# Kernel optimization log

Hardware: AMD Instinct MI355X
Metric: run time of the kernel (lower is better)

Reference implementation:

```python
import jax, jax.numpy as jnp
import numpy as np


def setup_inputs() -> dict:
    key = jax.random.key(0)
    ks = jax.random.split(key, 8)
    T, B, D = 2048, 8, 1024
    d, NM, k = 64, 8, 2
    Mp1 = NM + 1
    s_in = 1.0 / np.sqrt(D)
    X = jax.random.normal(ks[0], (T, B, D), dtype=jnp.float32)
    M0 = 0.02 * jax.random.normal(ks[1], (d, d), dtype=jnp.float32)
    W_q = s_in * jax.random.normal(ks[2], (D, d), dtype=jnp.float32)
    b_q = jnp.zeros((d,), jnp.float32)
    W_k = s_in * jax.random.normal(ks[3], (D, Mp1 * d), dtype=jnp.float32)
    b_k = jnp.zeros((Mp1 * d,), jnp.float32)
    W_v = s_in * jax.random.normal(ks[4], (D, Mp1 * d), dtype=jnp.float32)
    b_v = jnp.zeros((Mp1 * d,), jnp.float32)
    W_g = s_in * jax.random.normal(ks[5], (D, NM), dtype=jnp.float32)
    b_g = jnp.zeros((NM,), jnp.float32)
    return dict(X=X, M0=M0, W_q=W_q, b_q=b_q, W_k=W_k, b_k=b_k,
                W_v=W_v, b_v=b_v, W_g=W_g, b_g=b_g, k=k)


def _mom_forward(X, M0, W_q, b_q, W_k, b_k, W_v, b_v, W_g, b_g, k):
    T, B, D = X.shape
    d = M0.shape[0]
    NM = W_g.shape[1]
    Mp1 = NM + 1  # memory 0 is the always-on shared memory
    Kp1 = k + 1
    # --- gating + top-k memory selection ---
    scores = jax.nn.softmax(X @ W_g + b_g, axis=-1)               # (T,B,NM)
    m_sc, m_idx = jax.lax.top_k(scores, k)                        # (T,B,k)
    m_sc = m_sc / jnp.sum(m_sc, axis=-1, keepdims=True)
    m_idx = m_idx + 1                                             # shift: 0 reserved for shared memory
    idx_u = jnp.concatenate([jnp.zeros((T, B, 1), m_idx.dtype), m_idx], axis=2)  # (T,B,Kp1)
    sc_u = jnp.concatenate([jnp.ones((T, B, 1), m_sc.dtype), m_sc], axis=2)      # (T,B,Kp1)
    # --- varlen pack: sort replicated tokens by (batch, memory, time) ---
    # NB: the torch build_varlen_pack runs under @torch.no_grad -> detached
    t_rep = jnp.broadcast_to(jnp.arange(T)[:, None, None], (T, B, Kp1)).reshape(-1)
    b_rep = jnp.broadcast_to(jnp.arange(B)[None, :, None], (T, B, Kp1)).reshape(-1)
    m_rep = idx_u.reshape(-1)
    sort_key = b_rep * (Mp1 * T) + m_rep * T + t_rep              # unique per packed token
    perm = jnp.argsort(sort_key)
    t_o = t_rep[perm]
    b_o = b_rep[perm]
    m_id = m_rep[perm]
    alpha = jax.lax.stop_gradient(sc_u.reshape(-1)[perm])         # (Tt,)
    x_tilde = jax.lax.stop_gradient(
        jnp.broadcast_to(X[:, :, None, :], (T, B, Kp1, D)).reshape(-1, D)[perm])  # (Tt,D)
    Tt = T * B * Kp1
    # segment id per packed token; state resets at each new (batch, memory) segment
    seg = b_o * Mp1 + m_id
    new_seg = jnp.concatenate([jnp.ones((1,), bool), seg[1:] != seg[:-1]])
    # --- projections; pick k/v head matching each token's routed memory ---
    q_t = x_tilde @ W_q + b_q                                     # (Tt,d)
    K_all = (x_tilde @ W_k + b_k).reshape(Tt, Mp1, d)
    V_all = (x_tilde @ W_v + b_v).reshape(Tt, Mp1, d)
    k_t = jnp.take_along_axis(K_all, m_id[:, None, None], axis=1)[:, 0]  # (Tt,d)
    v_t = jnp.take_along_axis(V_all, m_id[:, None, None], axis=1)[:, 0]  # (Tt,d)
    # --- per-segment linear-attention recurrence: M_t = M0 + sum k_tau v_tau^T, o_t = q_t @ M_t ---
    def step(M, inp):
        qt, kt, vt, ns = inp
        M = jnp.where(ns, M0, M)
        M = M + kt[:, None] * vt[None, :]
        return M, qt @ M
    _, o_tilde = jax.lax.scan(step, M0, (q_t, k_t, v_t, new_seg))  # (Tt,d)
    # --- weighted scatter-add back to (T,B,d) ---
    o = jnp.zeros((T, B, d), X.dtype).at[t_o, b_o].add(alpha[:, None] * o_tilde)
    return o


def reference(X, M0, W_q, b_q, W_k, b_k, W_v, b_v, W_g, b_g, k):
    return _mom_forward(X, M0, W_q, b_q, W_k, b_k, W_v, b_v, W_g, b_g, k)
```

## Files before the change

### kernel.cpp

```cpp
#include <hip/hip_runtime.h>

#define TT   2048
#define BB   8
#define DD   1024
#define HD   64
#define MP1  9
#define NTOK (TT*BB)
#define CH   64
#define NC   32
#define NSEG (BB*MP1)
#define SEGCAP 2048
#define NCAT 1280
#define LDP  72
#define NZB  1024

typedef __attribute__((ext_vector_type(8))) short bf16x8;
typedef __attribute__((ext_vector_type(4))) float f32x4;

union U8 { uint4 v; unsigned short s[8]; };

static __device__ __forceinline__ unsigned short f2bf(float f) {
  union { float f; unsigned u; } c; c.f = f;
  unsigned r = (c.u + 0x7FFF + ((c.u >> 16) & 1)) >> 16;
  return (unsigned short)r;
}
static __device__ __forceinline__ float bf2f(unsigned short s) {
  union { unsigned u; float f; } c; c.u = ((unsigned)s) << 16;
  return c.f;
}

static __device__ __forceinline__ int sched_walk(
    const int* __restrict__ seglen, int bid, int* chunk_out) {
  const int batch = bid & 7;
  int idx = bid >> 3;
  for (int m = 0; m < MP1; m++) {
    int nch = (seglen[batch * MP1 + m] + 63) >> 6;
    if (idx < nch) { *chunk_out = idx; return batch * MP1 + m; }
    idx -= nch;
  }
  return -1;
}

__global__ __launch_bounds__(256) void prep(
    const float* __restrict__ X,
    const float* __restrict__ Wq, const float* __restrict__ Wk,
    const float* __restrict__ Wv, const float* __restrict__ bq,
    const float* __restrict__ bk, const float* __restrict__ bv,
    const float* __restrict__ Wg, const float* __restrict__ bg,
    unsigned short* __restrict__ Wt, float* __restrict__ bcat,
    int2* __restrict__ idxb, float2* __restrict__ alfb,
    unsigned short* __restrict__ Xb,
    float4* __restrict__ outz, int n4) {
  __shared__ float smem[8 * DD];
  const int tid = threadIdx.x;
  const int id = blockIdx.x;
  if (id >= 1344) {
    int i = (id - 1344) * 256 + tid;
    if (i < n4) outz[i] = make_float4(0.f, 0.f, 0.f, 0.f);
    return;
  }
  if (id < 320) {
    float (*tile)[65] = (float(*)[65])smem;
    const int n0 = (id % 20) * 64, k0 = (id / 20) * 64;
    const int c = tid & 63, rr = tid >> 6;
#pragma unroll 4
    for (int i = 0; i < 16; i++) {
      int kk = k0 + rr * 16 + i;
      int n  = n0 + c;
      float v = 0.f;
      if (n0 < 64)        v = Wq[kk * 64 + n];
      else if (n0 < 640)  v = Wk[kk * 576 + (n - 64)];
      else if (n0 < 1216) v = Wv[kk * 576 + (n - 640)];
      tile[rr * 16 + i][c] = v;
    }
    __syncthreads();
    const int lk = (tid & 15) * 4, ln = tid >> 4;
#pragma unroll
    for (int p = 0; p < 4; p++) {
      int nl = p * 16 + ln;
      ushort4 o;
      o.x = f2bf(tile[lk + 0][nl]); o.y = f2bf(tile[lk + 1][nl]);
      o.z = f2bf(tile[lk + 2][nl]); o.w = f2bf(tile[lk + 3][nl]);
      *(ushort4*)&Wt[(size_t)(n0 + nl) * DD + k0 + lk] = o;
    }
    if (id == 0) {
      for (int idx = tid; idx < NCAT; idx += 256) {
        float b = 0.f;
        if (idx < 64)        b = bq[idx];
        else if (idx < 640)  b = bk[idx - 64];
        else if (idx < 1216) b = bv[idx - 640];
        bcat[idx] = b;
      }
    }
    return;
  }
  float* wgT = smem;
#pragma unroll
  for (int idx4 = tid; idx4 < 2048; idx4 += 256) {
    float4 v = *(const float4*)&Wg[(size_t)idx4 * 4];
    int flat = idx4 * 4;
    int i = flat >> 3, j = flat & 7;
    wgT[(j + 0) * DD + i] = v.x;
    wgT[(j + 1) * DD + i] = v.y;
    wgT[(j + 2) * DD + i] = v.z;
    wgT[(j + 3) * DD + i] = v.w;
  }
  __syncthreads();
  const int lane = tid & 63, wave = tid >> 6;
  const int base_tok = (id - 320) * 16 + wave * 4;
  for (int tk = 0; tk < 4; tk++) {
    const int tok = base_tok + tk;
    const float* xr = X + (size_t)tok * DD;
    unsigned short* xbr = Xb + ((size_t)((tok & 7) * TT + (tok >> 3))) * DD;
    float p[8] = {0.f,0.f,0.f,0.f,0.f,0.f,0.f,0.f};
#pragma unroll
    for (int it = 0; it < 4; it++) {
      int i = it * 256 + lane * 4;
      float4 x = *(const float4*)&xr[i];
      ushort4 o;
      o.x = f2bf(x.x); o.y = f2bf(x.y); o.z = f2bf(x.z); o.w = f2bf(x.w);
      *(ushort4*)&xbr[i] = o;
#pragma unroll
      for (int j = 0; j < 8; j++) {
        float4 wv = *(const float4*)&wgT[j * DD + i];
        p[j] += x.x * wv.x + x.y * wv.y + x.z * wv.z + x.w * wv.w;
      }
    }
#pragma unroll
    for (int j = 0; j < 8; j++) {
      float v = p[j];
#pragma unroll
      for (int off = 32; off > 0; off >>= 1) v += __shfl_xor(v, off);
      p[j] = v + bg[j];
    }
    if (lane == 0) {
      int i1 = 0; float z1 = p[0];
#pragma unroll
      for (int j = 1; j < 8; j++) if (p[j] > z1) { z1 = p[j]; i1 = j; }
      int i2 = -1; float z2 = -3.0e38f;
#pragma unroll
      for (int j = 0; j < 8; j++) if (j != i1 && p[j] > z2) { z2 = p[j]; i2 = j; }
      float e   = expf(z2 - z1);
      float inv = 1.0f / (1.0f + e);
      idxb[tok] = make_int2(i1 + 1, i2 + 1);
      alfb[tok] = make_float2(inv, e * inv);
    }
  }
}

__global__ __launch_bounds__(1024) void pack_kernel(
    const int2* __restrict__ idxb, const float2* __restrict__ alfb,
    int* __restrict__ tlist, float* __restrict__ alist,
    int* __restrict__ seglen) {
  const int seg = blockIdx.x;
  const int b = seg / MP1, m = seg % MP1;
  const int tid = threadIdx.x;
  int* tl = tlist + (size_t)seg * SEGCAP;
  float* al = alist + (size_t)seg * SEGCAP;
  if (m == 0) {
    for (int pos = tid; pos < TT; pos += 1024) { tl[pos] = pos; al[pos] = 1.f; }
    if (tid == 0) seglen[seg] = TT;
    return;
  }
  __shared__ int wsum[16];
  const int lane = tid & 63, w = tid >> 6;
  int base = 0;
  for (int r = 0; r < TT / 1024; r++) {
    int t = r * 1024 + tid;
    int2 ix = idxb[t * BB + b];
    bool f = (ix.x == m || ix.y == m);
    float2 af = alfb[t * BB + b];
    float alpha = (ix.x == m) ? af.x : af.y;
    unsigned long long mask = __ballot(f);
    int lanepos = __popcll(mask & ((1ull << lane) - 1ull));
    if (lane == 0) wsum[w] = __popcll(mask);
    __syncthreads();
    int wbase = 0, total = 0;
#pragma unroll
    for (int i = 0; i < 16; i++) { int v = wsum[i]; if (i < w) wbase += v; total += v; }
    if (f) { int pos = base + wbase + lanepos; tl[pos] = t; al[pos] = alpha; }
    base += total;
    __syncthreads();
  }
  if (tid == 0) seglen[seg] = base;
  int Lpad = (base + 63) & ~63;
  for (int pos = base + tid; pos < Lpad; pos += 1024) { tl[pos] = 0; al[pos] = 0.f; }
}

#define ABUF_H 4096
#define BBUF_H 12288

template<bool DOQ>
static __device__ __forceinline__ void pkv_body(
    const unsigned short* __restrict__ Xb, const unsigned short* __restrict__ Wt,
    const float* __restrict__ bcat, const int* __restrict__ tlist,
    unsigned short* __restrict__ KVseg, unsigned short* __restrict__ Qd,
    unsigned short* Asb, unsigned short* Bsb, int* tls,
    int seg, int t0) {
  const int b = seg / MP1, m = seg % MP1;
  const int tid = threadIdx.x;
  const int lane = tid & 63, w = tid >> 6;
  if (tid < 64) tls[tid] = tlist[(size_t)seg * SEGCAP + t0 + tid];
  __syncthreads();

  const int lrow = lane >> 2;
  const int lk   = (lane & 3) * 8;
  const unsigned short* aPtr = Xb + ((size_t)b * TT + tls[w * 16 + lrow]) * DD + lk;
  const unsigned short* kPtr = Wt + (size_t)(64  + m * 64 + w * 16 + lrow) * DD + lk;
  const unsigned short* vPtr = Wt + (size_t)(640 + m * 64 + w * 16 + lrow) * DD + lk;
  const unsigned short* qPtr = Wt + (size_t)(w * 16 + lrow) * DD + lk;

  const int wr = (w >> 1) * 32;
  const int wc64 = (w & 1);
  const int quad = lane >> 4, l15 = lane & 15;

  float biasv[4], qbias[2];
#pragma unroll
  for (int n = 0; n < 4; n++) {
    int col = wc64 * 64 + n * 16 + l15;
    biasv[n] = bcat[col < 64 ? (64 + m * 64 + col) : (640 + m * 64 + (col - 64))];
  }
  if (DOQ) {
#pragma unroll
    for (int i = 0; i < 2; i++) qbias[i] = bcat[wc64 * 32 + i * 16 + l15];
  } else { qbias[0] = 0.f; qbias[1] = 0.f; }
  asm volatile("s_waitcnt vmcnt(0)" ::: "memory");
  __builtin_amdgcn_sched_barrier(0);

  f32x4 acc[2][4];
  f32x4 qacc[2][2];
#pragma unroll
  for (int i = 0; i < 2; i++) {
#pragma unroll
    for (int j = 0; j < 4; j++) acc[i][j] = (f32x4){0.f, 0.f, 0.f, 0.f};
#pragma unroll
    for (int j = 0; j < 2; j++) qacc[i][j] = (f32x4){0.f, 0.f, 0.f, 0.f};
  }

#define STG(BUF, K0)                                                             \
  do {                                                                           \
    unsigned short* As_ = Asb + (BUF) * ABUF_H;                                  \
    unsigned short* Bs_ = Bsb + (BUF) * BBUF_H;                                  \
    _Pragma("unroll")                                                            \
    for (int s = 0; s < 2; s++) {                                                \
      __builtin_amdgcn_global_load_lds(                                          \
          (const __attribute__((address_space(1))) unsigned int*)(aPtr + (K0) + s * 32), \
          (__attribute__((address_space(3))) unsigned int*)(As_ + s * 2048 + w * 512),   \
          16, 0, 0);                                                             \
      __builtin_amdgcn_global_load_lds(                                          \
          (const __attribute__((address_space(1))) unsigned int*)(kPtr + (K0) + s * 32), \
          (__attribute__((address_space(3))) unsigned int*)(Bs_ + s * 2048 + w * 512),   \
          16, 0, 0);                                                             \
      __builtin_amdgcn_global_load_lds(                                          \
          (const __attribute__((address_space(1))) unsigned int*)(vPtr + (K0) + s * 32), \
          (__attribute__((address_space(3))) unsigned int*)(Bs_ + 4096 + s * 2048 + w * 512), \
          16, 0, 0);                                                             \
      if (DOQ)                                                                   \
        __builtin_amdgcn_global_load_lds(                                        \
            (const __attribute__((address_space(1))) unsigned int*)(qPtr + (K0) + s * 32), \
            (__attribute__((address_space(3))) unsigned int*)(Bs_ + 8192 + s * 2048 + w * 512), \
            16, 0, 0);                                                           \
    }                                                                            \
  } while (0)

#define CMP(BUF)                                                                 \
  do {                                                                           \
    const unsigned short* As_ = Asb + (BUF) * ABUF_H;                            \
    const unsigned short* Bs_ = Bsb + (BUF) * BBUF_H;                            \
    _Pragma("unroll")                                                            \
    for (int s = 0; s < 2; s++) {                                                \
      bf16x8 af[2], bfr[4];                                                      \
      _Pragma("unroll")                                                          \
      for (int i = 0; i < 2; i++)                                                \
        af[i] = *(const bf16x8*)&As_[s * 2048 + (wr + i * 16 + l15) * 32 + quad * 8]; \
      _Pragma("unroll")                                                          \
      for (int n = 0; n < 4; n++)                                                \
        bfr[n] = *(const bf16x8*)&Bs_[wc64 * 4096 + s * 2048 + (n * 16 + l15) * 32 + quad * 8]; \
      _Pragma("unroll")                                                          \
      for (int mi = 0; mi < 2; mi++)                                             \
        _Pragma("unroll")                                                        \
        for (int ni = 0; ni < 4; ni++)                                           \
          acc[mi][ni] = __builtin_amdgcn_mfma_f32_16x16x32_bf16(af[mi], bfr[ni], acc[mi][ni], 0, 0, 0); \
      if (DOQ) {                                                                 \
        bf16x8 qf[2];                                                            \
        _Pragma("unroll")                                                        \
        for (int i = 0; i < 2; i++)                                              \
          qf[i] = *(const bf16x8*)&Bs_[8192 + s * 2048 + (wc64 * 32 + i * 16 + l15) * 32 + quad * 8]; \
        _Pragma("unroll")                                                        \
        for (int mi = 0; mi < 2; mi++)                                           \
          _Pragma("unroll")                                                      \
          for (int ni = 0; ni < 2; ni++)                                         \
            qacc[mi][ni] = __builtin_amdgcn_mfma_f32_16x16x32_bf16(af[mi], qf[ni], qacc[mi][ni], 0, 0, 0); \
      }                                                                          \
    }                                                                            \
  } while (0)

  STG(0, 0);
  STG(1, 64);
  for (int it = 0; it < 15; it++) {
    if (DOQ) asm volatile("s_waitcnt vmcnt(8)" ::: "memory");
    else     asm volatile("s_waitcnt vmcnt(6)" ::: "memory");
    __builtin_amdgcn_sched_barrier(0);
    asm volatile("s_barrier" ::: "memory");
    CMP(it & 1);
    asm volatile("s_waitcnt lgkmcnt(0)" ::: "memory");
    __builtin_amdgcn_sched_barrier(0);
    asm volatile("s_barrier" ::: "memory");
    if (it < 14) STG(it & 1, (it + 2) * 64);
  }
  asm volatile("s_waitcnt vmcnt(0)" ::: "memory");
  __builtin_amdgcn_sched_barrier(0);
  asm volatile("s_barrier" ::: "memory");
  CMP(1);
#undef STG
#undef CMP

#pragma unroll
  for (int ni = 0; ni < 4; ni++) {
    int col = wc64 * 64 + ni * 16 + l15;
#pragma unroll
    for (int mi = 0; mi < 2; mi++) {
      int p = t0 + wr + mi * 16 + quad * 4;
#pragma unroll
      for (int r = 0; r < 4; r++) {
        float v = acc[mi][ni][r] + biasv[ni];
        KVseg[((size_t)seg * SEGCAP + p + r) * 128 + col] = f2bf(v);
      }
    }
  }
  if (DOQ) {
#pragma unroll
    for (int ni = 0; ni < 2; ni++) {
      int qcol = wc64 * 32 + ni * 16 + l15;
#pragma unroll
      for (int mi = 0; mi < 2; mi++) {
        int pr = wr + mi * 16 + quad * 4;
#pragma unroll
        for (int r = 0; r < 4; r++) {
          int t = tls[pr + r];
          float v = qacc[mi][ni][r] + qbias[ni];
          Qd[(size_t)(t * BB + b) * HD + qcol] = f2bf(v);
        }
      }
    }
  }
}

__global__ __launch_bounds__(256) void pkv_mfma(
    const unsigned short* __restrict__ Xb, const unsigned short* __restrict__ Wt,
    const float* __restrict__ bcat,
    const int* __restrict__ tlist, const int* __restrict__ seglen,
    unsigned short* __restrict__ KVseg, unsigned short* __restrict__ Qd) {
  int chunk;
  const int seg = sched_walk(seglen, blockIdx.x, &chunk);
  if (seg < 0) return;
  const int t0 = chunk * 64;
  __shared__ unsigned short Asb[2 * ABUF_H];
  __shared__ unsigned short Bsb[2 * BBUF_H];
  __shared__ int tls[64];
  if (seg % MP1 == 0)
    pkv_body<true>(Xb, Wt, bcat, tlist, KVseg, Qd, Asb, Bsb, tls, seg, t0);
  else
    pkv_body<false>(Xb, Wt, bcat, tlist, KVseg, Qd, Asb, Bsb, tls, seg, t0);
}

__global__ __launch_bounds__(256) void chunk_intra(
    const unsigned short* __restrict__ Qd, const unsigned short* __restrict__ KVseg,
    const int* __restrict__ tlist, const float* __restrict__ alist,
    const int* __restrict__ seglen,
    unsigned short* __restrict__ Sb16, float* __restrict__ out) {
  int chunk;
  const int seg = sched_walk(seglen, blockIdx.x, &chunk);
  if (seg < 0) return;
  const int L = seglen[seg];
  const int t0 = chunk * CH;
  __shared__ unsigned short Qs[64 * LDP];
  __shared__ unsigned short Ks[64 * LDP];
  __shared__ unsigned short KTs[64 * LDP];
  __shared__ unsigned short VTs[64 * LDP];
  const int b = seg / MP1;
  const int tid = threadIdx.x;
  const int* tl = tlist + (size_t)seg * SEGCAP;
  {
    int row = tid >> 2, c16 = (tid & 3) << 4;
    int pos = t0 + row;
    int t = tl[pos];
    const unsigned short* qb = Qd + (size_t)(t * BB + b) * HD;
    *(uint4*)&Qs[row * LDP + c16]     = *(const uint4*)(qb + c16);
    *(uint4*)&Qs[row * LDP + c16 + 8] = *(const uint4*)(qb + c16 + 8);
    const unsigned short* kvb = KVseg + ((size_t)seg * SEGCAP + pos) * 128;
    U8 k0, k1, v0, v1;
    k0.v = *(const uint4*)(kvb + c16);
    k1.v = *(const uint4*)(kvb + c16 + 8);
    v0.v = *(const uint4*)(kvb + 64 + c16);
    v1.v = *(const uint4*)(kvb + 64 + c16 + 8);
    if (pos >= L) { uint4 z = {0,0,0,0}; k0.v = z; k1.v = z; }
    *(uint4*)&Ks[row * LDP + c16]     = k0.v;
    *(uint4*)&Ks[row * LDP + c16 + 8] = k1.v;
#pragma unroll
    for (int j = 0; j < 8; j++) {
      KTs[(c16 + j) * LDP + row]     = k0.s[j];
      KTs[(c16 + 8 + j) * LDP + row] = k1.s[j];
      VTs[(c16 + j) * LDP + row]     = v0.s[j];
      VTs[(c16 + 8 + j) * LDP + row] = v1.s[j];
    }
  }
  __syncthreads();
  const int lane = tid & 63, w = tid >> 6;
  const int quad = lane >> 4, l15 = lane & 15;
  {
    const unsigned short* arow = &VTs[(w * 16 + l15) * LDP];
    bf16x8 a0 = *(const bf16x8*)(arow + quad * 8);
    bf16x8 a1 = *(const bf16x8*)(arow + 32 + quad * 8);
    unsigned short* Sp = Sb16 + ((size_t)seg * NC + chunk) * 4096;
#pragma unroll
    for (int n = 0; n < 4; n++) {
      const unsigned short* brow = &KTs[(n * 16 + l15) * LDP];
      f32x4 acc = __builtin_amdgcn_mfma_f32_16x16x32_bf16(a0, *(const bf16x8*)(brow + quad * 8),
                                                          (f32x4){0.f,0.f,0.f,0.f}, 0, 0, 0);
      acc = __builtin_amdgcn_mfma_f32_16x16x32_bf16(a1, *(const bf16x8*)(brow + 32 + quad * 8),
                                                    acc, 0, 0, 0);
#pragma unroll
      for (int r = 0; r < 4; r++)
        Sp[(w * 16 + quad * 4 + r) * 64 + n * 16 + l15] = f2bf(acc[r]);
    }
  }
  unsigned short* qrow = &Qs[(w * 16 + l15) * LDP];
  bf16x8 aq0 = *(const bf16x8*)(qrow + quad * 8);
  bf16x8 aq1 = *(const bf16x8*)(qrow + 32 + quad * 8);
  f32x4 pp[4];
#pragma unroll
  for (int n = 0; n < 4; n++) {
    const unsigned short* krow = &Ks[(n * 16 + l15) * LDP];
    pp[n] = __builtin_amdgcn_mfma_f32_16x16x32_bf16(aq0, *(const bf16x8*)(krow + quad * 8),
                                                    (f32x4){0.f,0.f,0.f,0.f}, 0, 0, 0);
    pp[n] = __builtin_amdgcn_mfma_f32_16x16x32_bf16(aq1, *(const bf16x8*)(krow + 32 + quad * 8),
                                                    pp[n], 0, 0, 0);
  }
#pragma unroll
  for (int n = 0; n < 4; n++)
#pragma unroll
    for (int r = 0; r < 4; r++) {
      int i = w * 16 + quad * 4 + r, j = n * 16 + l15;
      Qs[i * LDP + j] = (j <= i) ? f2bf(pp[n][r]) : (unsigned short)0;
    }
  bf16x8 ap0 = *(const bf16x8*)(qrow + quad * 8);
  bf16x8 ap1 = *(const bf16x8*)(qrow + 32 + quad * 8);
  f32x4 po[4];
#pragma unroll
  for (int n = 0; n < 4; n++) {
    const unsigned short* vrow = &VTs[(n * 16 + l15) * LDP];
    po[n] = __builtin_amdgcn_mfma_f32_16x16x32_bf16(ap0, *(const bf16x8*)(vrow + quad * 8),
                                                    (f32x4){0.f,0.f,0.f,0.f}, 0, 0, 0);
    po[n] = __builtin_amdgcn_mfma_f32_16x16x32_bf16(ap1, *(const bf16x8*)(vrow + 32 + quad * 8),
                                                    po[n], 0, 0, 0);
  }
#pragma unroll
  for (int r = 0; r < 4; r++) {
    int pos = t0 + w * 16 + quad * 4 + r;
    if (pos < L) {
      int t = tl[pos];
      float alpha = alist[(size_t)seg * SEGCAP + pos];
#pragma unroll
      for (int n = 0; n < 4; n++)
        atomicAdd(&out[(size_t)(t * BB + b) * HD + n * 16 + l15], alpha * po[n][r]);
    }
  }
}

__global__ __launch_bounds__(256) void scan_kernel(
    const float* __restrict__ M0, const int* __restrict__ seglen,
    unsigned short* __restrict__ Sb16) {
  const int batch = blockIdx.x & 7;
  const int idx = blockIdx.x >> 3;
  const int seg = batch * MP1 + (idx >> 2), slab = idx & 3;
  const int nch = (seglen[seg] + CH - 1) / CH;
  if (nch <= 0) return;
  const int tid = threadIdx.x;
  const int off = slab * 1024 + tid * 4;
  float run[4];
#pragma unroll
  for (int u = 0; u < 4; u++) {
    int o = off + u;
    run[u] = M0[(o & 63) * 64 + (o >> 6)];
  }
  unsigned short* base = Sb16 + (size_t)seg * NC * 4096;
  ushort4 s = *(const ushort4*)(base + off);
  for (int c = 0; c < nch; c++) {
    unsigned short* p = base + c * 4096 + off;
    ushort4 snext;
    if (c + 1 < nch) snext = *(const ushort4*)(p + 4096);
    ushort4 o;
    o.x = f2bf(run[0]); o.y = f2bf(run[1]); o.z = f2bf(run[2]); o.w = f2bf(run[3]);
    *(ushort4*)p = o;
    run[0] += bf2f(s.x); run[1] += bf2f(s.y); run[2] += bf2f(s.z); run[3] += bf2f(s.w);
    s = snext;
  }
}

__global__ __launch_bounds__(256) void chunk_inter(
    const unsigned short* __restrict__ Qd, const unsigned short* __restrict__ Sb16,
    const int* __restrict__ tlist, const float* __restrict__ alist,
    const int* __restrict__ seglen, float* __restrict__ out) {
  int chunk;
  const int seg = sched_walk(seglen, blockIdx.x, &chunk);
  if (seg < 0) return;
  const int L = seglen[seg];
  const int t0 = chunk * CH;
  __shared__ unsigned short Qs[64 * LDP];
  __shared__ unsigned short MT[64 * LDP];
  const int b = seg / MP1;
  const int tid = threadIdx.x;
  const int* tl = tlist + (size_t)seg * SEGCAP;
  {
    int row = tid >> 2, c16 = (tid & 3) << 4;
    int pos = t0 + row;
    const unsigned short* qb = Qd + (size_t)(tl[pos] * BB + b) * HD;
    *(uint4*)&Qs[row * LDP + c16]     = *(const uint4*)(qb + c16);
    *(uint4*)&Qs[row * LDP + c16 + 8] = *(const uint4*)(qb + c16 + 8);
    const unsigned short* Mp = Sb16 + ((size_t)seg * NC + chunk) * 4096 + row * 64 + c16;
    *(uint4*)&MT[row * LDP + c16]     = *(const uint4*)(Mp);
    *(uint4*)&MT[row * LDP + c16 + 8] = *(const uint4*)(Mp + 8);
  }
  __syncthreads();
  const int lane = tid & 63, w = tid >> 6;
  const int quad = lane >> 4, l15 = lane & 15;
  const unsigned short* qrow = &Qs[(w * 16 + l15) * LDP];
  bf16x8 aq0 = *(const bf16x8*)(qrow + quad * 8);
  bf16x8 aq1 = *(const bf16x8*)(qrow + 32 + quad * 8);
  f32x4 po[4];
#pragma unroll
  for (int n = 0; n < 4; n++) {
    const unsigned short* mrow = &MT[(n * 16 + l15) * LDP];
    po[n] = __builtin_amdgcn_mfma_f32_16x16x32_bf16(aq0, *(const bf16x8*)(mrow + quad * 8),
                                                    (f32x4){0.f,0.f,0.f,0.f}, 0, 0, 0);
    po[n] = __builtin_amdgcn_mfma_f32_16x16x32_bf16(aq1, *(const bf16x8*)(mrow + 32 + quad * 8),
                                                    po[n], 0, 0, 0);
  }
#pragma unroll
  for (int r = 0; r < 4; r++) {
    int pos = t0 + w * 16 + quad * 4 + r;
    if (pos < L) {
      int t = tl[pos];
      float alpha = alist[(size_t)seg * SEGCAP + pos];
#pragma unroll
      for (int n = 0; n < 4; n++)
        atomicAdd(&out[(size_t)(t * BB + b) * HD + n * 16 + l15], alpha * po[n][r]);
    }
  }
}

extern "C" void kernel_launch(void* const* d_in, const int* in_sizes, int n_in,
                              void* d_out, int out_size, void* d_ws, size_t ws_size,
                              hipStream_t stream) {
  const float* X  = (const float*)d_in[0];
  const float* M0 = (const float*)d_in[1];
  const float* Wq = (const float*)d_in[2];
  const float* bq = (const float*)d_in[3];
  const float* Wk = (const float*)d_in[4];
  const float* bk = (const float*)d_in[5];
  const float* Wv = (const float*)d_in[6];
  const float* bv = (const float*)d_in[7];
  const float* Wg = (const float*)d_in[8];
  const float* bg = (const float*)d_in[9];

  char* ws = (char*)d_ws;
  unsigned short* Xb   = (unsigned short*)(ws);
  unsigned short* Wt   = (unsigned short*)(ws + 33554432ULL);
  float*          bcat = (float*)         (ws + 36175872ULL);
  unsigned short* Qd   = (unsigned short*)(ws + 36180992ULL);
  unsigned short* KVsg = (unsigned short*)(ws + 38278144ULL);
  unsigned short* Sb16 = (unsigned short*)(ws + 76026880ULL);
  int2*           idxb = (int2*)          (ws + 94901248ULL);
  float2*         alfb = (float2*)        (ws + 95032320ULL);
  int*            tlist= (int*)           (ws + 95163392ULL);
  float*          alist= (float*)         (ws + 95753216ULL);
  int*            slen = (int*)           (ws + 96343040ULL);

  float* out = (float*)d_out;
  const int n4 = out_size / 4;

  prep<<<320 + NTOK / 16 + NZB, 256, 0, stream>>>(
      X, Wq, Wk, Wv, bq, bk, bv, Wg, bg, Wt, bcat, idxb, alfb, Xb,
      (float4*)out, n4);
  pack_kernel<<<NSEG, 1024, 0, stream>>>(idxb, alfb, tlist, alist, slen);
  pkv_mfma<<<1024, 256, 0, stream>>>(Xb, Wt, bcat, tlist, slen, KVsg, Qd);
  chunk_intra<<<1024, 256, 0, stream>>>(Qd, KVsg, tlist, alist, slen, Sb16, out);
  scan_kernel<<<288, 256, 0, stream>>>(M0, slen, Sb16);
  chunk_inter<<<1024, 256, 0, stream>>>(Qd, Sb16, tlist, alist, slen, out);
}
```

Before: 112.4 us.

## Fuse K/V/Q projection into intra-chunk attention kernel, drop KV global round trip

Merges the projection kernel and the intra-chunk kernel into one, so projected K, V and Q tiles go straight from MFMA accumulators into shared memory instead of through a global KV buffer. Every segment now computes the Q projection locally, which adds Q-weight loads and MFMAs for non-shared memories, and Q is still written to global only for memory 0. This removes one launch and the KV write/read traffic, but raises per-block work and LDS reuse pressure.

```diff
diff --git a/kernel.cpp b/kernel.cpp
--- a/kernel.cpp
+++ b/kernel.cpp
@@ -190,14 +190,23 @@
 #define ABUF_H 4096
 #define BBUF_H 12288
 
-template<bool DOQ>
-static __device__ __forceinline__ void pkv_body(
+__global__ __launch_bounds__(256) void pkv_intra(
     const unsigned short* __restrict__ Xb, const unsigned short* __restrict__ Wt,
-    const float* __restrict__ bcat, const int* __restrict__ tlist,
-    unsigned short* __restrict__ KVseg, unsigned short* __restrict__ Qd,
-    unsigned short* Asb, unsigned short* Bsb, int* tls,
-    int seg, int t0) {
+    const float* __restrict__ bcat,
+    const int* __restrict__ tlist, const float* __restrict__ alist,
+    const int* __restrict__ seglen,
+    unsigned short* __restrict__ Sb16, unsigned short* __restrict__ Qd,
+    float* __restrict__ out) {
+  int chunk;
+  const int seg = sched_walk(seglen, blockIdx.x, &chunk);
+  if (seg < 0) return;
+  const int t0 = chunk * 64;
+  const int L = seglen[seg];
   const int b = seg / MP1, m = seg % MP1;
+  __shared__ unsigned short lds[2 * (ABUF_H + BBUF_H)];
+  __shared__ int tls[64];
+  unsigned short* Asb = lds;
+  unsigned short* Bsb = lds + 2 * ABUF_H;
   const int tid = threadIdx.x;
   const int lane = tid & 63, w = tid >> 6;
   if (tid < 64) tls[tid] = tlist[(size_t)seg * SEGCAP + t0 + tid];
@@ -220,10 +229,8 @@
     int col = wc64 * 64 + n * 16 + l15;
     biasv[n] = bcat[col < 64 ? (64 + m * 64 + col) : (640 + m * 64 + (col - 64))];
   }
-  if (DOQ) {
-#pragma unroll
-    for (int i = 0; i < 2; i++) qbias[i] = bcat[wc64 * 32 + i * 16 + l15];
-  } else { qbias[0] = 0.f; qbias[1] = 0.f; }
+#pragma unroll
+  for (int i = 0; i < 2; i++) qbias[i] = bcat[wc64 * 32 + i * 16 + l15];
   asm volatile("s_waitcnt vmcnt(0)" ::: "memory");
   __builtin_amdgcn_sched_barrier(0);
 
@@ -255,11 +262,10 @@
           (const __attribute__((address_space(1))) unsigned int*)(vPtr + (K0) + s * 32), \
           (__attribute__((address_space(3))) unsigned int*)(Bs_ + 4096 + s * 2048 + w * 512), \
           16, 0, 0);                                                             \
-      if (DOQ)                                                                   \
-        __builtin_amdgcn_global_load_lds(                                        \
-            (const __attribute__((address_space(1))) unsigned int*)(qPtr + (K0) + s * 32), \
-            (__attribute__((address_space(3))) unsigned int*)(Bs_ + 8192 + s * 2048 + w * 512), \
-            16, 0, 0);                                                           \
+      __builtin_amdgcn_global_load_lds(                                          \
+          (const __attribute__((address_space(1))) unsigned int*)(qPtr + (K0) + s * 32), \
+          (__attribute__((address_space(3))) unsigned int*)(Bs_ + 8192 + s * 2048 + w * 512), \
+          16, 0, 0);                                                             \
     }                                                                            \
   } while (0)
 
@@ -281,7 +287,7 @@
         _Pragma("unroll")                                                        \
         for (int ni = 0; ni < 4; ni++)                                           \
           acc[mi][ni] = __builtin_amdgcn_mfma_f32_16x16x32_bf16(af[mi], bfr[ni], acc[mi][ni], 0, 0, 0); \
-      if (DOQ) {                                                                 \
+      {                                                                          \
         bf16x8 qf[2];                                                            \
         _Pragma("unroll")                                                        \
         for (int i = 0; i < 2; i++)                                              \
@@ -298,8 +304,7 @@
   STG(0, 0);
   STG(1, 64);
   for (int it = 0; it < 15; it++) {
-    if (DOQ) asm volatile("s_waitcnt vmcnt(8)" ::: "memory");
-    else     asm volatile("s_waitcnt vmcnt(6)" ::: "memory");
+    asm volatile("s_waitcnt vmcnt(8)" ::: "memory");
     __builtin_amdgcn_sched_barrier(0);
     asm volatile("s_barrier" ::: "memory");
     CMP(it & 1);
@@ -315,99 +320,51 @@
 #undef STG
 #undef CMP
 
+  asm volatile("s_waitcnt lgkmcnt(0)" ::: "memory");
+  __builtin_amdgcn_sched_barrier(0);
+  __syncthreads();
+
+  unsigned short* Qs  = lds;
+  unsigned short* Ks  = lds + 64 * LDP;
+  unsigned short* KTs = lds + 2 * 64 * LDP;
+  unsigned short* VTs = lds + 3 * 64 * LDP;
+
+#pragma unroll
+  for (int ni = 0; ni < 2; ni++) {
+    int qcol = wc64 * 32 + ni * 16 + l15;
+#pragma unroll
+    for (int mi = 0; mi < 2; mi++) {
+#pragma unroll
+      for (int r = 0; r < 4; r++) {
+        int pr = wr + mi * 16 + quad * 4 + r;
+        unsigned short qv = f2bf(qacc[mi][ni][r] + qbias[ni]);
+        Qs[pr * LDP + qcol] = qv;
+        if (m == 0) Qd[(size_t)((t0 + pr) * BB + b) * HD + qcol] = qv;
+      }
+    }
+  }
 #pragma unroll
   for (int ni = 0; ni < 4; ni++) {
-    int col = wc64 * 64 + ni * 16 + l15;
+    int col = ni * 16 + l15;
 #pragma unroll
     for (int mi = 0; mi < 2; mi++) {
-      int p = t0 + wr + mi * 16 + quad * 4;
 #pragma unroll
       for (int r = 0; r < 4; r++) {
-        float v = acc[mi][ni][r] + biasv[ni];
-        KVseg[((size_t)seg * SEGCAP + p + r) * 128 + col] = f2bf(v);
-      }
-    }
-  }
-  if (DOQ) {
-#pragma unroll
-    for (int ni = 0; ni < 2; ni++) {
-      int qcol = wc64 * 32 + ni * 16 + l15;
-#pragma unroll
-      for (int mi = 0; mi < 2; mi++) {
-        int pr = wr + mi * 16 + quad * 4;
-#pragma unroll
-        for (int r = 0; r < 4; r++) {
-          int t = tls[pr + r];
-          float v = qacc[mi][ni][r] + qbias[ni];
-          Qd[(size_t)(t * BB + b) * HD + qcol] = f2bf(v);
+        int pr = wr + mi * 16 + quad * 4 + r;
+        unsigned short v = f2bf(acc[mi][ni][r] + biasv[ni]);
+        if (wc64 == 0) {
+          unsigned short kv = (t0 + pr < L) ? v : (unsigned short)0;
+          Ks[pr * LDP + col]  = kv;
+          KTs[col * LDP + pr] = kv;
+        } else {
+          VTs[col * LDP + pr] = v;
         }
       }
     }
   }
-}
-
-__global__ __launch_bounds__(256) void pkv_mfma(
-    const unsigned short* __restrict__ Xb, const unsigned short* __restrict__ Wt,
-    const float* __restrict__ bcat,
-    const int* __restrict__ tlist, const int* __restrict__ seglen,
-    unsigned short* __restrict__ KVseg, unsigned short* __restrict__ Qd) {
-  int chunk;
-  const int seg = sched_walk(seglen, blockIdx.x, &chunk);
-  if (seg < 0) return;
-  const int t0 = chunk * 64;
-  __shared__ unsigned short Asb[2 * ABUF_H];
-  __shared__ unsigned short Bsb[2 * BBUF_H];
-  __shared__ int tls[64];
-  if (seg % MP1 == 0)
-    pkv_body<true>(Xb, Wt, bcat, tlist, KVseg, Qd, Asb, Bsb, tls, seg, t0);
-  else
-    pkv_body<false>(Xb, Wt, bcat, tlist, KVseg, Qd, Asb, Bsb, tls, seg, t0);
-}
-
-__global__ __launch_bounds__(256) void chunk_intra(
-    const unsigned short* __restrict__ Qd, const unsigned short* __restrict__ KVseg,
-    const int* __restrict__ tlist, const float* __restrict__ alist,
-    const int* __restrict__ seglen,
-    unsigned short* __restrict__ Sb16, float* __restrict__ out) {
-  int chunk;
-  const int seg = sched_walk(seglen, blockIdx.x, &chunk);
-  if (seg < 0) return;
-  const int L = seglen[seg];
-  const int t0 = chunk * CH;
-  __shared__ unsigned short Qs[64 * LDP];
-  __shared__ unsigned short Ks[64 * LDP];
-  __shared__ unsigned short KTs[64 * LDP];
-  __shared__ unsigned short VTs[64 * LDP];
-  const int b = seg / MP1;
-  const int tid = threadIdx.x;
+  __syncthreads();
+
   const int* tl = tlist + (size_t)seg * SEGCAP;
-  {
-    int row = tid >> 2, c16 = (tid & 3) << 4;
-    int pos = t0 + row;
-    int t = tl[pos];
-    const unsigned short* qb = Qd + (size_t)(t * BB + b) * HD;
-    *(uint4*)&Qs[row * LDP + c16]     = *(const uint4*)(qb + c16);
-    *(uint4*)&Qs[row * LDP + c16 + 8] = *(const uint4*)(qb + c16 + 8);
-    const unsigned short* kvb = KVseg + ((size_t)seg * SEGCAP + pos) * 128;
-    U8 k0, k1, v0, v1;
-    k0.v = *(const uint4*)(kvb + c16);
-    k1.v = *(const uint4*)(kvb + c16 + 8);
-    v0.v = *(const uint4*)(kvb + 64 + c16);
-    v1.v = *(const uint4*)(kvb + 64 + c16 + 8);
-    if (pos >= L) { uint4 z = {0,0,0,0}; k0.v = z; k1.v = z; }
-    *(uint4*)&Ks[row * LDP + c16]     = k0.v;
-    *(uint4*)&Ks[row * LDP + c16 + 8] = k1.v;
-#pragma unroll
-    for (int j = 0; j < 8; j++) {
-      KTs[(c16 + j) * LDP + row]     = k0.s[j];
-      KTs[(c16 + 8 + j) * LDP + row] = k1.s[j];
-      VTs[(c16 + j) * LDP + row]     = v0.s[j];
-      VTs[(c16 + 8 + j) * LDP + row] = v1.s[j];
-    }
-  }
-  __syncthreads();
-  const int lane = tid & 63, w = tid >> 6;
-  const int quad = lane >> 4, l15 = lane & 15;
   {
     const unsigned short* arow = &VTs[(w * 16 + l15) * LDP];
     bf16x8 a0 = *(const bf16x8*)(arow + quad * 8);
@@ -416,13 +373,13 @@
 #pragma unroll
     for (int n = 0; n < 4; n++) {
       const unsigned short* brow = &KTs[(n * 16 + l15) * LDP];
-      f32x4 acc = __builtin_amdgcn_mfma_f32_16x16x32_bf16(a0, *(const bf16x8*)(brow + quad * 8),
-                                                          (f32x4){0.f,0.f,0.f,0.f}, 0, 0, 0);
-      acc = __builtin_amdgcn_mfma_f32_16x16x32_bf16(a1, *(const bf16x8*)(brow + 32 + quad * 8),
-                                                    acc, 0, 0, 0);
+      f32x4 a2 = __builtin_amdgcn_mfma_f32_16x16x32_bf16(a0, *(const bf16x8*)(brow + quad * 8),
+                                                         (f32x4){0.f,0.f,0.f,0.f}, 0, 0, 0);
+      a2 = __builtin_amdgcn_mfma_f32_16x16x32_bf16(a1, *(const bf16x8*)(brow + 32 + quad * 8),
+                                                   a2, 0, 0, 0);
 #pragma unroll
       for (int r = 0; r < 4; r++)
-        Sp[(w * 16 + quad * 4 + r) * 64 + n * 16 + l15] = f2bf(acc[r]);
+        Sp[(w * 16 + quad * 4 + r) * 64 + n * 16 + l15] = f2bf(a2[r]);
     }
   }
   unsigned short* qrow = &Qs[(w * 16 + l15) * LDP];
@@ -569,7 +526,6 @@
   unsigned short* Wt   = (unsigned short*)(ws + 33554432ULL);
   float*          bcat = (float*)         (ws + 36175872ULL);
   unsigned short* Qd   = (unsigned short*)(ws + 36180992ULL);
-  unsigned short* KVsg = (unsigned short*)(ws + 38278144ULL);
   unsigned short* Sb16 = (unsigned short*)(ws + 76026880ULL);
   int2*           idxb = (int2*)          (ws + 94901248ULL);
   float2*         alfb = (float2*)        (ws + 95032320ULL);
@@ -584,8 +540,7 @@
       X, Wq, Wk, Wv, bq, bk, bv, Wg, bg, Wt, bcat, idxb, alfb, Xb,
       (float4*)out, n4);
   pack_kernel<<<NSEG, 1024, 0, stream>>>(idxb, alfb, tlist, alist, slen);
-  pkv_mfma<<<1024, 256, 0, stream>>>(Xb, Wt, bcat, tlist, slen, KVsg, Qd);
-  chunk_intra<<<1024, 256, 0, stream>>>(Qd, KVsg, tlist, alist, slen, Sb16, out);
+  pkv_intra<<<1024, 256, 0, stream>>>(Xb, Wt, bcat, tlist, alist, slen, Sb16, Qd, out);
   scan_kernel<<<288, 256, 0, stream>>>(M0, slen, Sb16);
   chunk_inter<<<1024, 256, 0, stream>>>(Qd, Sb16, tlist, alist, slen, out);
 }
```

Result: no change. 111.6 us (median of 2 runs) (-0.7%).
